# Kernel optimization log

Measured on AMD Instinct MI355X. Metric: run time of the kernel, lower is better.

The kernel has to match this reference:

```python
import jax, jax.numpy as jnp
import numpy as np
import math

B, M, C = 256, 256, 1024
ALPHA = 0.1

def setup_inputs() -> dict:
    key = jax.random.key(0)
    k1, k2 = jax.random.split(key)
    input_encoded = jax.random.normal(k1, (B, C), dtype=jnp.float32)
    memory_mean = jax.random.normal(k2, (M, C), dtype=jnp.float32)
    return {"input_encoded": input_encoded, "memory_mean": memory_mean}

def reference(input_encoded, memory_mean):
    b, c = input_encoded.shape
    m = memory_mean.shape[0]
    # ---- write_to_memory ----
    # similarity of each input with each prior memory slot: [B, M]
    sims = jnp.einsum('bc,mc->bm', input_encoded, memory_mean)
    closest_idx = jnp.argmax(sims, axis=1)                      # [B]
    sel = memory_mean[closest_idx]                              # [B, C]
    new_row = (1.0 - ALPHA) * sel + ALPHA * input_encoded       # [B, C]
    onehot = (jnp.arange(m)[None, :] == closest_idx[:, None])   # [B, M] bool
    mem = jnp.broadcast_to(memory_mean[None], (b, m, c))
    updated_memory = jnp.where(onehot[:, :, None], new_row[:, None, :], mem)  # [B, M, C]
    dkl_write = 0.5 * jnp.sum((input_encoded - sel) ** 2, axis=1)             # [B]
    # ---- read_with_encoded_input ----
    scale = 1.0 / math.sqrt(c)
    scores = jnp.einsum('bc,bmc->bm', input_encoded, updated_memory) * scale  # [B, M]
    attn = jax.nn.softmax(scores, axis=1)
    z_read = jnp.einsum('bm,bmc->bc', attn, updated_memory)                   # [B, C]
    dkl_read = 0.5 * jnp.sum((z_read - input_encoded) ** 2, axis=1)           # [B]
    kl_div = dkl_write + dkl_read
    return z_read, updated_memory, kl_div
```

## Files before the change

### kernel.cpp

```cpp
#include <hip/hip_runtime.h>
#include <math.h>

#define B_DIM 256
#define M_DIM 256
#define C_DIM 1024
#define C4    256
#define UM_OFF (B_DIM * C_DIM)
#define KL_OFF (UM_OFF + B_DIM * M_DIM * C_DIM)
#define SCALE  0.03125f

typedef float nfloat4 __attribute__((ext_vector_type(4)));

__device__ __forceinline__ void nt_store4(float4 v, nfloat4* p) {
    nfloat4 n = {v.x, v.y, v.z, v.w};
    __builtin_nontemporal_store(n, p);
}

__global__ __launch_bounds__(256) void tm_stream(const float* __restrict__ x,
                                                 const float* __restrict__ mem,
                                                 float* __restrict__ out) {
    const int b = blockIdx.x;
    const int q = blockIdx.y;
    const int t = threadIdx.x;
    const int lane = t & 63;
    const int wv = t >> 6;

    __shared__ float4 s_x[C4];
    s_x[t] = ((const float4*)(x + (size_t)b * C_DIM))[t];
    __syncthreads();
    const float4 xr0 = s_x[lane];
    const float4 xr1 = s_x[lane + 64];
    const float4 xr2 = s_x[lane + 128];
    const float4 xr3 = s_x[lane + 192];

    const float4* mem4 = (const float4*)mem;
    nfloat4* um4 = (nfloat4*)(out + UM_OFF) + (size_t)b * M_DIM * C4;
    float* simsrow = out + (size_t)b * C_DIM;

    const int m0 = (q << 5) | (wv << 3);
    #pragma unroll
    for (int i = 0; i < 8; ++i) {
        const int m = m0 + i;
        const float4* mr = mem4 + (size_t)m * C4;
        float4 a0 = mr[lane];
        float4 a1 = mr[lane + 64];
        float4 a2 = mr[lane + 128];
        float4 a3 = mr[lane + 192];
        float p0 = a0.x*xr0.x + a0.y*xr0.y + a0.z*xr0.z + a0.w*xr0.w;
        float p1 = a1.x*xr1.x + a1.y*xr1.y + a1.z*xr1.z + a1.w*xr1.w;
        float p2 = a2.x*xr2.x + a2.y*xr2.y + a2.z*xr2.z + a2.w*xr2.w;
        float p3 = a3.x*xr3.x + a3.y*xr3.y + a3.z*xr3.z + a3.w*xr3.w;
        float acc = (p0 + p1) + (p2 + p3);
        #pragma unroll
        for (int off = 32; off; off >>= 1) acc += __shfl_xor(acc, off, 64);
        nfloat4* dst = um4 + (size_t)m * C4;
        nt_store4(a0, dst + lane);
        nt_store4(a1, dst + lane + 64);
        nt_store4(a2, dst + lane + 128);
        nt_store4(a3, dst + lane + 192);
        if (lane == 0) simsrow[m] = acc;
    }
}

__device__ __forceinline__ float4 bsum4(float4 v, float4* s_w, int lane, int wv) {
    #pragma unroll
    for (int off = 32; off; off >>= 1) {
        v.x += __shfl_xor(v.x, off, 64);
        v.y += __shfl_xor(v.y, off, 64);
        v.z += __shfl_xor(v.z, off, 64);
        v.w += __shfl_xor(v.w, off, 64);
    }
    if (lane == 0) s_w[wv] = v;
    __syncthreads();
    float4 r = s_w[0];
    #pragma unroll
    for (int w = 1; w < 8; ++w) {
        r.x += s_w[w].x; r.y += s_w[w].y; r.z += s_w[w].z; r.w += s_w[w].w;
    }
    __syncthreads();
    return r;
}

__device__ __forceinline__ float4 bmax4(float4 v, float4* s_w, int lane, int wv) {
    #pragma unroll
    for (int off = 32; off; off >>= 1) {
        v.x = fmaxf(v.x, __shfl_xor(v.x, off, 64));
        v.y = fmaxf(v.y, __shfl_xor(v.y, off, 64));
        v.z = fmaxf(v.z, __shfl_xor(v.z, off, 64));
        v.w = fmaxf(v.w, __shfl_xor(v.w, off, 64));
    }
    if (lane == 0) s_w[wv] = v;
    __syncthreads();
    float4 r = s_w[0];
    #pragma unroll
    for (int w = 1; w < 8; ++w) {
        r.x = fmaxf(r.x, s_w[w].x); r.y = fmaxf(r.y, s_w[w].y);
        r.z = fmaxf(r.z, s_w[w].z); r.w = fmaxf(r.w, s_w[w].w);
    }
    __syncthreads();
    return r;
}

__global__ __launch_bounds__(512) void tm_finish(const float* __restrict__ x,
                                                 const float* __restrict__ mem,
                                                 float* __restrict__ out) {
    const int g = blockIdx.x;
    const int t = threadIdx.x;
    const int lane = t & 63;
    const int wv = t >> 6;
    const int tc = t & 255;
    const int h  = t >> 8;

    __shared__ float4 s_x[4][C4];
    __shared__ float  s_sims[4][M_DIM];
    __shared__ float4 s_d[4][C4];
    __shared__ float  s_attn[4][M_DIM];
    __shared__ float4 s_zp[4][C4];
    __shared__ float4 s_w4[8];
    __shared__ float  s_av[8];
    __shared__ int    s_ai[8];
    __shared__ int    s_idx[4];

    const float4* mem4 = (const float4*)mem;

    #pragma unroll
    for (int j = 0; j < 4; ++j) {
        const int b = (g << 2) + j;
        if (h == 0) s_x[j][tc] = ((const float4*)(x + (size_t)b * C_DIM))[tc];
        else        s_sims[j][tc] = out[(size_t)b * C_DIM + tc];
    }
    __syncthreads();

    float4 pv = make_float4(0.f, 0.f, 0.f, 0.f);
    if (h == 0) {
        float4 x0 = s_x[0][tc], x1 = s_x[1][tc], x2 = s_x[2][tc], x3 = s_x[3][tc];
        pv.x = x0.x*x0.x + x0.y*x0.y + x0.z*x0.z + x0.w*x0.w;
        pv.y = x1.x*x1.x + x1.y*x1.y + x1.z*x1.z + x1.w*x1.w;
        pv.z = x2.x*x2.x + x2.y*x2.y + x2.z*x2.z + x2.w*x2.w;
        pv.w = x3.x*x3.x + x3.y*x3.y + x3.z*x3.z + x3.w*x3.w;
    }
    float4 n2v = bsum4(pv, s_w4, lane, wv);
    const float n2_[4] = {n2v.x, n2v.y, n2v.z, n2v.w};

    #pragma unroll
    for (int j = 0; j < 4; ++j) {
        float av = -INFINITY; int ai = 0x7fffffff;
        if (h == 0) { av = s_sims[j][tc]; ai = tc; }
        #pragma unroll
        for (int off = 32; off; off >>= 1) {
            float ov = __shfl_xor(av, off, 64);
            int   oi = __shfl_xor(ai, off, 64);
            if (ov > av || (ov == av && oi < ai)) { av = ov; ai = oi; }
        }
        if (lane == 0) { s_av[wv] = av; s_ai[wv] = ai; }
        __syncthreads();
        if (t == 0) {
            float bv = s_av[0]; int bi = s_ai[0];
            #pragma unroll
            for (int w = 1; w < 8; ++w) {
                float v2 = s_av[w]; int i2 = s_ai[w];
                if (v2 > bv || (v2 == bv && i2 < bi)) { bv = v2; bi = i2; }
            }
            s_idx[j] = bi;
        }
        __syncthreads();
    }

    float4 dwp = make_float4(0.f, 0.f, 0.f, 0.f);
    #pragma unroll
    for (int j = 0; j < 4; ++j) {
        const int b = (g << 2) + j;
        const int idx = s_idx[j];
        if (h == 0) {
            float4 sl = mem4[(size_t)idx * C4 + tc];
            float4 xv = s_x[j][tc];
            float4 d = make_float4(xv.x - sl.x, xv.y - sl.y, xv.z - sl.z, xv.w - sl.w);
            s_d[j][tc] = d;
            float dd = d.x*d.x + d.y*d.y + d.z*d.z + d.w*d.w;
            if      (j == 0) dwp.x = dd;
            else if (j == 1) dwp.y = dd;
            else if (j == 2) dwp.z = dd;
            else             dwp.w = dd;
            float4 bl = make_float4(0.9f*sl.x + 0.1f*xv.x, 0.9f*sl.y + 0.1f*xv.y,
                                    0.9f*sl.z + 0.1f*xv.z, 0.9f*sl.w + 0.1f*xv.w);
            nt_store4(bl, (nfloat4*)(out + UM_OFF) + ((size_t)b * M_DIM + idx) * C4 + tc);
        }
    }
    float4 dwv = bsum4(dwp, s_w4, lane, wv);
    const float dw_[4] = {dwv.x, dwv.y, dwv.z, dwv.w};

    float4 scv = make_float4(-INFINITY, -INFINITY, -INFINITY, -INFINITY);
    if (h == 0) {
        #pragma unroll
        for (int j = 0; j < 4; ++j) {
            const int idx = s_idx[j];
            float sc = (tc == idx) ? (0.9f * s_sims[j][idx] + 0.1f * n2_[j]) * SCALE
                                   : s_sims[j][tc] * SCALE;
            if      (j == 0) scv.x = sc;
            else if (j == 1) scv.y = sc;
            else if (j == 2) scv.z = sc;
            else             scv.w = sc;
        }
    }
    float4 mxv = bmax4(scv, s_w4, lane, wv);
    float4 ev = make_float4(0.f, 0.f, 0.f, 0.f);
    if (h == 0) {
        ev.x = expf(scv.x - mxv.x);
        ev.y = expf(scv.y - mxv.y);
        ev.z = expf(scv.z - mxv.z);
        ev.w = expf(scv.w - mxv.w);
    }
    float4 esv = bsum4(ev, s_w4, lane, wv);
    if (h == 0) {
        s_attn[0][tc] = ev.x / esv.x;
        s_attn[1][tc] = ev.y / esv.y;
        s_attn[2][tc] = ev.z / esv.z;
        s_attn[3][tc] = ev.w / esv.w;
    }
    __syncthreads();

    float4 z0 = make_float4(0.f,0.f,0.f,0.f), z1 = z0, z2 = z0, z3 = z0;
    #pragma unroll 4
    for (int i = 0; i < 128; ++i) {
        const int m = (h << 7) + i;
        float4 v = mem4[(size_t)m * C4 + tc];
        const float a0 = s_attn[0][m], a1 = s_attn[1][m];
        const float a2 = s_attn[2][m], a3 = s_attn[3][m];
        z0.x = fmaf(a0, v.x, z0.x); z0.y = fmaf(a0, v.y, z0.y);
        z0.z = fmaf(a0, v.z, z0.z); z0.w = fmaf(a0, v.w, z0.w);
        z1.x = fmaf(a1, v.x, z1.x); z1.y = fmaf(a1, v.y, z1.y);
        z1.z = fmaf(a1, v.z, z1.z); z1.w = fmaf(a1, v.w, z1.w);
        z2.x = fmaf(a2, v.x, z2.x); z2.y = fmaf(a2, v.y, z2.y);
        z2.z = fmaf(a2, v.z, z2.z); z2.w = fmaf(a2, v.w, z2.w);
        z3.x = fmaf(a3, v.x, z3.x); z3.y = fmaf(a3, v.y, z3.y);
        z3.z = fmaf(a3, v.z, z3.z); z3.w = fmaf(a3, v.w, z3.w);
    }
    if (h == 1) { s_zp[0][tc] = z0; s_zp[1][tc] = z1; s_zp[2][tc] = z2; s_zp[3][tc] = z3; }
    __syncthreads();

    float4 drp = make_float4(0.f, 0.f, 0.f, 0.f);
    if (h == 0) {
        float4 o0 = s_zp[0][tc], o1 = s_zp[1][tc], o2 = s_zp[2][tc], o3 = s_zp[3][tc];
        z0.x += o0.x; z0.y += o0.y; z0.z += o0.z; z0.w += o0.w;
        z1.x += o1.x; z1.y += o1.y; z1.z += o1.z; z1.w += o1.w;
        z2.x += o2.x; z2.y += o2.y; z2.z += o2.z; z2.w += o2.w;
        z3.x += o3.x; z3.y += o3.y; z3.z += o3.z; z3.w += o3.w;
        const float ax0 = s_attn[0][s_idx[0]] * 0.1f;
        const float ax1 = s_attn[1][s_idx[1]] * 0.1f;
        const float ax2 = s_attn[2][s_idx[2]] * 0.1f;
        const float ax3 = s_attn[3][s_idx[3]] * 0.1f;
        float4 d0 = s_d[0][tc], d1 = s_d[1][tc], d2 = s_d[2][tc], d3 = s_d[3][tc];
        z0.x = fmaf(ax0, d0.x, z0.x); z0.y = fmaf(ax0, d0.y, z0.y);
        z0.z = fmaf(ax0, d0.z, z0.z); z0.w = fmaf(ax0, d0.w, z0.w);
        z1.x = fmaf(ax1, d1.x, z1.x); z1.y = fmaf(ax1, d1.y, z1.y);
        z1.z = fmaf(ax1, d1.z, z1.z); z1.w = fmaf(ax1, d1.w, z1.w);
        z2.x = fmaf(ax2, d2.x, z2.x); z2.y = fmaf(ax2, d2.y, z2.y);
        z2.z = fmaf(ax2, d2.z, z2.z); z2.w = fmaf(ax2, d2.w, z2.w);
        z3.x = fmaf(ax3, d3.x, z3.x); z3.y = fmaf(ax3, d3.y, z3.y);
        z3.z = fmaf(ax3, d3.z, z3.z); z3.w = fmaf(ax3, d3.w, z3.w);
        float4 x0 = s_x[0][tc], x1 = s_x[1][tc], x2 = s_x[2][tc], x3 = s_x[3][tc];
        float e0x = z0.x-x0.x, e0y = z0.y-x0.y, e0z = z0.z-x0.z, e0w = z0.w-x0.w;
        float e1x = z1.x-x1.x, e1y = z1.y-x1.y, e1z = z1.z-x1.z, e1w = z1.w-x1.w;
        float e2x = z2.x-x2.x, e2y = z2.y-x2.y, e2z = z2.z-x2.z, e2w = z2.w-x2.w;
        float e3x = z3.x-x3.x, e3y = z3.y-x3.y, e3z = z3.z-x3.z, e3w = z3.w-x3.w;
        drp.x = e0x*e0x + e0y*e0y + e0z*e0z + e0w*e0w;
        drp.y = e1x*e1x + e1y*e1y + e1z*e1z + e1w*e1w;
        drp.z = e2x*e2x + e2y*e2y + e2z*e2z + e2w*e2w;
        drp.w = e3x*e3x + e3y*e3y + e3z*e3z + e3w*e3w;
        float4* zout = (float4*)out;
        zout[((size_t)((g << 2) + 0)) * C4 + tc] = z0;
        zout[((size_t)((g << 2) + 1)) * C4 + tc] = z1;
        zout[((size_t)((g << 2) + 2)) * C4 + tc] = z2;
        zout[((size_t)((g << 2) + 3)) * C4 + tc] = z3;
    }
    float4 drv = bsum4(drp, s_w4, lane, wv);
    if (t == 0) {
        out[KL_OFF + (g << 2) + 0] = 0.5f * (dw_[0] + drv.x);
        out[KL_OFF + (g << 2) + 1] = 0.5f * (dw_[1] + drv.y);
        out[KL_OFF + (g << 2) + 2] = 0.5f * (dw_[2] + drv.z);
        out[KL_OFF + (g << 2) + 3] = 0.5f * (dw_[3] + drv.w);
    }
}

extern "C" void kernel_launch(void* const* d_in, const int* in_sizes, int n_in,
                              void* d_out, int out_size, void* d_ws, size_t ws_size,
                              hipStream_t stream) {
    const float* x   = (const float*)d_in[0];
    const float* mem = (const float*)d_in[1];
    float* out = (float*)d_out;

    tm_stream<<<dim3(B_DIM, 8), dim3(256), 0, stream>>>(x, mem, out);
    tm_finish<<<dim3(64), dim3(512), 0, stream>>>(x, mem, out);
}
```

Measured before the change: 69.54 us.

## Compute similarities in finish kernel first, then stream updated memory with blended row

Moves the similarity GEMV into the first kernel, which now computes sims, argmax, softmax and z_read for 4 batch rows per block and writes the argmax indices to workspace. The broadcast kernel now runs second. It loads 8 memory rows once, reuses them across 4 batch rows, and writes the blended row in place. This removes the separate scattered overwrite and lets each memory load serve several output rows. In exchange the small first kernel now does the dot products itself with only 64 blocks, which could serialize latency before the bandwidth-bound store phase.

```diff
diff --git a/kernel.cpp b/kernel.cpp
--- a/kernel.cpp
+++ b/kernel.cpp
@@ -11,55 +11,13 @@
 
 typedef float nfloat4 __attribute__((ext_vector_type(4)));
 
-__device__ __forceinline__ void nt_store4(float4 v, nfloat4* p) {
+__device__ __forceinline__ void nt_store4(float4 v, float4* p) {
     nfloat4 n = {v.x, v.y, v.z, v.w};
-    __builtin_nontemporal_store(n, p);
-}
-
-__global__ __launch_bounds__(256) void tm_stream(const float* __restrict__ x,
-                                                 const float* __restrict__ mem,
-                                                 float* __restrict__ out) {
-    const int b = blockIdx.x;
-    const int q = blockIdx.y;
-    const int t = threadIdx.x;
-    const int lane = t & 63;
-    const int wv = t >> 6;
-
-    __shared__ float4 s_x[C4];
-    s_x[t] = ((const float4*)(x + (size_t)b * C_DIM))[t];
-    __syncthreads();
-    const float4 xr0 = s_x[lane];
-    const float4 xr1 = s_x[lane + 64];
-    const float4 xr2 = s_x[lane + 128];
-    const float4 xr3 = s_x[lane + 192];
-
-    const float4* mem4 = (const float4*)mem;
-    nfloat4* um4 = (nfloat4*)(out + UM_OFF) + (size_t)b * M_DIM * C4;
-    float* simsrow = out + (size_t)b * C_DIM;
-
-    const int m0 = (q << 5) | (wv << 3);
-    #pragma unroll
-    for (int i = 0; i < 8; ++i) {
-        const int m = m0 + i;
-        const float4* mr = mem4 + (size_t)m * C4;
-        float4 a0 = mr[lane];
-        float4 a1 = mr[lane + 64];
-        float4 a2 = mr[lane + 128];
-        float4 a3 = mr[lane + 192];
-        float p0 = a0.x*xr0.x + a0.y*xr0.y + a0.z*xr0.z + a0.w*xr0.w;
-        float p1 = a1.x*xr1.x + a1.y*xr1.y + a1.z*xr1.z + a1.w*xr1.w;
-        float p2 = a2.x*xr2.x + a2.y*xr2.y + a2.z*xr2.z + a2.w*xr2.w;
-        float p3 = a3.x*xr3.x + a3.y*xr3.y + a3.z*xr3.z + a3.w*xr3.w;
-        float acc = (p0 + p1) + (p2 + p3);
-        #pragma unroll
-        for (int off = 32; off; off >>= 1) acc += __shfl_xor(acc, off, 64);
-        nfloat4* dst = um4 + (size_t)m * C4;
-        nt_store4(a0, dst + lane);
-        nt_store4(a1, dst + lane + 64);
-        nt_store4(a2, dst + lane + 128);
-        nt_store4(a3, dst + lane + 192);
-        if (lane == 0) simsrow[m] = acc;
-    }
+    __builtin_nontemporal_store(n, (nfloat4*)p);
+}
+
+__device__ __forceinline__ float dot4(float4 a, float4 b) {
+    return a.x*b.x + a.y*b.y + a.z*b.z + a.w*b.w;
 }
 
 __device__ __forceinline__ float4 bsum4(float4 v, float4* s_w, int lane, int wv) {
@@ -101,9 +59,10 @@
     return r;
 }
 
-__global__ __launch_bounds__(512) void tm_finish(const float* __restrict__ x,
-                                                 const float* __restrict__ mem,
-                                                 float* __restrict__ out) {
+__global__ __launch_bounds__(512) void tm_pre(const float* __restrict__ x,
+                                              const float* __restrict__ mem,
+                                              float* __restrict__ out,
+                                              int* __restrict__ idx_ws) {
     const int g = blockIdx.x;
     const int t = threadIdx.x;
     const int lane = t & 63;
@@ -127,17 +86,45 @@
     for (int j = 0; j < 4; ++j) {
         const int b = (g << 2) + j;
         if (h == 0) s_x[j][tc] = ((const float4*)(x + (size_t)b * C_DIM))[tc];
-        else        s_sims[j][tc] = out[(size_t)b * C_DIM + tc];
+    }
+    __syncthreads();
+
+    {
+        const float4 x00 = s_x[0][lane], x01 = s_x[0][lane+64], x02 = s_x[0][lane+128], x03 = s_x[0][lane+192];
+        const float4 x10 = s_x[1][lane], x11 = s_x[1][lane+64], x12 = s_x[1][lane+128], x13 = s_x[1][lane+192];
+        const float4 x20 = s_x[2][lane], x21 = s_x[2][lane+64], x22 = s_x[2][lane+128], x23 = s_x[2][lane+192];
+        const float4 x30 = s_x[3][lane], x31 = s_x[3][lane+64], x32 = s_x[3][lane+128], x33 = s_x[3][lane+192];
+        for (int i = 0; i < 32; ++i) {
+            const int m = (wv << 5) | i;
+            const float4* mr = mem4 + ((size_t)m << 8);
+            float4 a0 = mr[lane];
+            float4 a1 = mr[lane + 64];
+            float4 a2 = mr[lane + 128];
+            float4 a3 = mr[lane + 192];
+            float p0 = dot4(a0,x00) + dot4(a1,x01) + dot4(a2,x02) + dot4(a3,x03);
+            float p1 = dot4(a0,x10) + dot4(a1,x11) + dot4(a2,x12) + dot4(a3,x13);
+            float p2 = dot4(a0,x20) + dot4(a1,x21) + dot4(a2,x22) + dot4(a3,x23);
+            float p3 = dot4(a0,x30) + dot4(a1,x31) + dot4(a2,x32) + dot4(a3,x33);
+            #pragma unroll
+            for (int off = 32; off; off >>= 1) {
+                p0 += __shfl_xor(p0, off, 64);
+                p1 += __shfl_xor(p1, off, 64);
+                p2 += __shfl_xor(p2, off, 64);
+                p3 += __shfl_xor(p3, off, 64);
+            }
+            if (lane == 0) {
+                s_sims[0][m] = p0; s_sims[1][m] = p1;
+                s_sims[2][m] = p2; s_sims[3][m] = p3;
+            }
+        }
     }
     __syncthreads();
 
     float4 pv = make_float4(0.f, 0.f, 0.f, 0.f);
     if (h == 0) {
         float4 x0 = s_x[0][tc], x1 = s_x[1][tc], x2 = s_x[2][tc], x3 = s_x[3][tc];
-        pv.x = x0.x*x0.x + x0.y*x0.y + x0.z*x0.z + x0.w*x0.w;
-        pv.y = x1.x*x1.x + x1.y*x1.y + x1.z*x1.z + x1.w*x1.w;
-        pv.z = x2.x*x2.x + x2.y*x2.y + x2.z*x2.z + x2.w*x2.w;
-        pv.w = x3.x*x3.x + x3.y*x3.y + x3.z*x3.z + x3.w*x3.w;
+        pv.x = dot4(x0, x0); pv.y = dot4(x1, x1);
+        pv.z = dot4(x2, x2); pv.w = dot4(x3, x3);
     }
     float4 n2v = bsum4(pv, s_w4, lane, wv);
     const float n2_[4] = {n2v.x, n2v.y, n2v.z, n2v.w};
@@ -165,25 +152,22 @@
         }
         __syncthreads();
     }
+    if (t < 4) idx_ws[(g << 2) + t] = s_idx[t];
 
     float4 dwp = make_float4(0.f, 0.f, 0.f, 0.f);
     #pragma unroll
     for (int j = 0; j < 4; ++j) {
-        const int b = (g << 2) + j;
         const int idx = s_idx[j];
         if (h == 0) {
-            float4 sl = mem4[(size_t)idx * C4 + tc];
+            float4 sl = mem4[((size_t)idx << 8) + tc];
             float4 xv = s_x[j][tc];
             float4 d = make_float4(xv.x - sl.x, xv.y - sl.y, xv.z - sl.z, xv.w - sl.w);
             s_d[j][tc] = d;
-            float dd = d.x*d.x + d.y*d.y + d.z*d.z + d.w*d.w;
+            float dd = dot4(d, d);
             if      (j == 0) dwp.x = dd;
             else if (j == 1) dwp.y = dd;
             else if (j == 2) dwp.z = dd;
             else             dwp.w = dd;
-            float4 bl = make_float4(0.9f*sl.x + 0.1f*xv.x, 0.9f*sl.y + 0.1f*xv.y,
-                                    0.9f*sl.z + 0.1f*xv.z, 0.9f*sl.w + 0.1f*xv.w);
-            nt_store4(bl, (nfloat4*)(out + UM_OFF) + ((size_t)b * M_DIM + idx) * C4 + tc);
         }
     }
     float4 dwv = bsum4(dwp, s_w4, lane, wv);
@@ -223,7 +207,7 @@
     #pragma unroll 4
     for (int i = 0; i < 128; ++i) {
         const int m = (h << 7) + i;
-        float4 v = mem4[(size_t)m * C4 + tc];
+        float4 v = mem4[((size_t)m << 8) + tc];
         const float a0 = s_attn[0][m], a1 = s_attn[1][m];
         const float a2 = s_attn[2][m], a3 = s_attn[3][m];
         z0.x = fmaf(a0, v.x, z0.x); z0.y = fmaf(a0, v.y, z0.y);
@@ -282,13 +266,54 @@
     }
 }
 
+__global__ __launch_bounds__(256) void tm_stream(const float* __restrict__ x,
+                                                 const float* __restrict__ mem,
+                                                 const int* __restrict__ idx_ws,
+                                                 float* __restrict__ out_um) {
+    const int mx = blockIdx.x;
+    const int bg = blockIdx.y;
+    const int t  = threadIdx.x;
+    const int m0 = mx << 3;
+    const int b0 = bg << 2;
+
+    const float4* mem4 = (const float4*)mem;
+    float4* um4 = (float4*)out_um;
+
+    float4 r[8];
+    #pragma unroll
+    for (int i = 0; i < 8; ++i)
+        r[i] = mem4[((size_t)(m0 + i) << 8) + t];
+
+    #pragma unroll
+    for (int j = 0; j < 4; ++j) {
+        const int b = b0 + j;
+        const int li = idx_ws[b] - m0;
+        float4 xv = make_float4(0.f, 0.f, 0.f, 0.f);
+        if (li >= 0 && li < 8)
+            xv = ((const float4*)(x + (size_t)b * C_DIM))[t];
+        float4* dst = um4 + (((size_t)(b << 8) | m0) << 8) + t;
+        #pragma unroll
+        for (int i = 0; i < 8; ++i) {
+            float4 v = r[i];
+            if (i == li) {
+                v.x = 0.9f*v.x + 0.1f*xv.x;
+                v.y = 0.9f*v.y + 0.1f*xv.y;
+                v.z = 0.9f*v.z + 0.1f*xv.z;
+                v.w = 0.9f*v.w + 0.1f*xv.w;
+            }
+            nt_store4(v, dst + ((size_t)i << 8));
+        }
+    }
+}
+
 extern "C" void kernel_launch(void* const* d_in, const int* in_sizes, int n_in,
                               void* d_out, int out_size, void* d_ws, size_t ws_size,
                               hipStream_t stream) {
     const float* x   = (const float*)d_in[0];
     const float* mem = (const float*)d_in[1];
     float* out = (float*)d_out;
-
-    tm_stream<<<dim3(B_DIM, 8), dim3(256), 0, stream>>>(x, mem, out);
-    tm_finish<<<dim3(64), dim3(512), 0, stream>>>(x, mem, out);
-}
+    int* idx_ws = (int*)d_ws;
+
+    tm_pre<<<dim3(64), dim3(512), 0, stream>>>(x, mem, out, idx_ws);
+    tm_stream<<<dim3(32, 64), dim3(256), 0, stream>>>(x, mem, idx_ws, out + UM_OFF);
+}
```

Result: slower. 95.69 us (+37.6%).
